# Kernel tuning notes

Hardware: AMD Instinct MI355X
Metric: run time of the kernel (lower is better)

The kernel has to match this reference:

```python
import jax, jax.numpy as jnp
import numpy as np

B, Z, NOBS = 16384, 64, 2
D = Z + NOBS  # update_mlp_in_size
H1, H2 = 16, 16
HC1, HC2 = 32, 32


def setup_inputs() -> dict:
    key = jax.random.key(0)
    ks = jax.random.split(key, 20)
    inp = {}
    inp['latents'] = jax.random.normal(ks[0], (B, Z), jnp.float32)
    inp['obs'] = jax.random.normal(ks[1], (B, NOBS), jnp.float32)
    # reparameterization noise (torch.randn_like equivalents, made explicit)
    inp['noise_update'] = jax.random.normal(ks[2], (B, D, Z), jnp.float32)
    inp['noise_global'] = jax.random.normal(ks[3], (B, Z), jnp.float32)
    # parameters
    inp['z_0'] = jax.random.normal(ks[4], (Z,), jnp.float32)
    inp['mult_u'] = jnp.ones((D, Z), jnp.float32)
    inp['logvar_u'] = jax.random.uniform(ks[5], (D, Z), jnp.float32, -3.0, -2.0)
    inp['mult_g'] = jnp.ones((Z,), jnp.float32)
    inp['logvar_g'] = jax.random.uniform(ks[6], (Z,), jnp.float32, -3.0, -2.0)
    # per-latent update MLPs, batched over Z
    s = lambda fan_in: 1.0 / np.sqrt(fan_in)
    inp['W1'] = jax.random.uniform(ks[7], (Z, D, H1), jnp.float32, -s(D), s(D))
    inp['b1'] = jax.random.uniform(ks[8], (Z, H1), jnp.float32, -s(D), s(D))
    inp['W2'] = jax.random.uniform(ks[9], (Z, H1, H2), jnp.float32, -s(H1), s(H1))
    inp['b2'] = jax.random.uniform(ks[10], (Z, H2), jnp.float32, -s(H1), s(H1))
    inp['W3'] = jax.random.uniform(ks[11], (Z, H2, 2), jnp.float32, -s(H2), s(H2))
    inp['b3'] = jax.random.uniform(ks[12], (Z, 2), jnp.float32, -s(H2), s(H2))
    # choice MLP (include_stimulus=False -> input dim Z)
    inp['Wc1'] = jax.random.uniform(ks[13], (Z, HC1), jnp.float32, -s(Z), s(Z))
    inp['bc1'] = jax.random.uniform(ks[14], (HC1,), jnp.float32, -s(Z), s(Z))
    inp['Wc2'] = jax.random.uniform(ks[15], (HC1, HC2), jnp.float32, -s(HC1), s(HC1))
    inp['bc2'] = jax.random.uniform(ks[16], (HC2,), jnp.float32, -s(HC1), s(HC1))
    inp['Wc3'] = jax.random.uniform(ks[17], (HC2, 2), jnp.float32, -s(HC2), s(HC2))
    inp['bc3'] = jax.random.uniform(ks[18], (2,), jnp.float32, -s(HC2), s(HC2))
    inp['t_0'] = 0  # False
    return inp


def reference(latents, obs, noise_update, noise_global, z_0, mult_u, logvar_u,
              mult_g, logvar_g, W1, b1, W2, b2, W3, b3,
              Wc1, bc1, Wc2, bc2, Wc3, bc3, t_0):
    lat = jnp.broadcast_to(z_0, latents.shape) if t_0 else latents  # [B,Z]
    x = jnp.concatenate([lat, obs], axis=-1)  # [B,D]
    # --- per-latent update bottlenecks, vectorized over Z ---
    var_u = jnp.exp(logvar_u)                      # [D,Z]
    mean_u = x[:, :, None] * mult_u[None]          # [B,D,Z]
    kld_u = -0.5 * jnp.sum(1.0 + logvar_u[None] - mean_u ** 2 - var_u[None], axis=1)  # [B,Z]
    x_tilde = noise_update * jnp.sqrt(var_u)[None] + mean_u  # [B,D,Z]
    # --- per-latent tiny MLPs, batched as grouped GEMMs ---
    h = jax.nn.relu(jnp.einsum('bdz,zdh->bzh', x_tilde, W1) + b1[None])
    h = jax.nn.relu(jnp.einsum('bzh,zhk->bzk', h, W2) + b2[None])
    o = jnp.einsum('bzk,zko->bzo', h, W3) + b3[None]          # [B,Z,2]
    u = o[..., 0]
    w = jax.nn.sigmoid(o[..., 1])
    new_latents = (1.0 - w) * lat + u * w          # gated update, [B,Z]
    # --- global bottleneck ---
    var_g = jnp.exp(logvar_g)
    mean_g = mult_g * new_latents
    kld_g = -0.5 * jnp.sum(1.0 + logvar_g - mean_g ** 2 - var_g, axis=-1)  # [B]
    z_tilde = noise_global * jnp.sqrt(var_g) + mean_g
    # --- choice MLP (no stimulus) ---
    y = jax.nn.relu(z_tilde @ Wc1 + bc1)
    y = jax.nn.relu(y @ Wc2 + bc2)
    y = y @ Wc3 + bc3                              # [B,2]
    return (y, z_tilde, kld_g, kld_u)
```

## Files before the change

kernel.cpp:

```cpp
#include <hip/hip_runtime.h>
#include <hip/hip_bf16.h>
#include <stdint.h>

#define BB 16384
#define ZZ 64
#define DD 66
#define NB 4
#define WPB 4

#define OFF_SVMU 0
#define OFF_C0U  8448
#define OFF_MG   8512
#define OFF_SVG  8576
#define OFF_C0G  8640

__global__ void prep_kernel(const float* __restrict__ mult_u, const float* __restrict__ logvar_u,
                            const float* __restrict__ mult_g, const float* __restrict__ logvar_g,
                            float* __restrict__ ws) {
  const int t = threadIdx.x;
  for (int i = t; i < DD*ZZ; i += 256) {
    ws[OFF_SVMU + 2*i]     = mult_u[i];
    ws[OFF_SVMU + 2*i + 1] = __expf(0.5f * logvar_u[i]);
  }
  if (t < ZZ) {
    float s = 0.f;
    for (int d = 0; d < DD; ++d) {
      const float lv = logvar_u[d*ZZ + t];
      s += 1.f + lv - __expf(lv);
    }
    ws[OFF_C0U + t] = -0.5f * s;
    ws[OFF_MG  + t] = mult_g[t];
    ws[OFF_SVG + t] = __expf(0.5f * logvar_g[t]);
  }
  if (t == 0) {
    float s = 0.f;
    for (int z = 0; z < ZZ; ++z) {
      const float lv = logvar_g[z];
      s += 1.f + lv - __expf(lv);
    }
    ws[OFF_C0G] = -0.5f * s;
  }
}

__global__ __launch_bounds__(256, 2)
void disrnn_main(const float* __restrict__ latents, const float* __restrict__ obs,
                 const float* __restrict__ noise_u, const float* __restrict__ noise_g,
                 const float* __restrict__ z0, const float* __restrict__ W1,
                 const float* __restrict__ b1, const float* __restrict__ W2,
                 const float* __restrict__ b2, const float* __restrict__ W3,
                 const float* __restrict__ b3,
                 const float* __restrict__ ws, const int* __restrict__ t0p,
                 float* __restrict__ out) {
  float* out_zt = out + BB*2;
  float* out_kg = out + BB*2 + BB*ZZ;
  float* out_ku = out + BB*2 + BB*ZZ + BB;

  __shared__ float x_lds[WPB][NB][68];
  __shared__ float red[WPB][NB][64];

  const int tid  = threadIdx.x;
  const int w    = tid >> 6;
  const int lane = tid & 63;
  const int b0   = (blockIdx.x * WPB + w) * NB;
  const int t0   = *t0p;

  const float c0u_l = ws[OFF_C0U + lane];
  const float mg_l  = ws[OFF_MG + lane];
  const float svg_l = ws[OFF_SVG + lane];
  const float c0g   = ws[OFF_C0G];
  const float b3_0  = b3[lane*2];
  const float b3_1  = b3[lane*2 + 1];
  const float2* __restrict__ svmu = (const float2*)(ws + OFF_SVMU);

#pragma unroll
  for (int i = 0; i < NB; ++i) {
    x_lds[w][i][lane] = t0 ? z0[lane] : latents[(b0 + i)*ZZ + lane];
    if (lane < 2) x_lds[w][i][ZZ + lane] = obs[(b0 + i)*2 + lane];
  }
  __syncthreads();

  float acc[NB][16], kacc[NB];
  {
    const float4* bp = reinterpret_cast<const float4*>(b1 + lane*16);
    float b1r[16];
#pragma unroll
    for (int q = 0; q < 4; ++q) {
      const float4 v = bp[q];
      b1r[4*q] = v.x; b1r[4*q+1] = v.y; b1r[4*q+2] = v.z; b1r[4*q+3] = v.w;
    }
#pragma unroll
    for (int i = 0; i < NB; ++i) {
      kacc[i] = 0.f;
#pragma unroll
      for (int h = 0; h < 16; ++h) acc[i][h] = b1r[h];
    }
  }

  for (int d = 0; d < DD; ++d) {
    const float2 sm = svmu[d*ZZ + lane];
    const float4* wp = reinterpret_cast<const float4*>(W1 + (lane*DD + d)*16);
    float wv[16];
#pragma unroll
    for (int q = 0; q < 4; ++q) {
      const float4 v = wp[q];
      wv[4*q] = v.x; wv[4*q+1] = v.y; wv[4*q+2] = v.z; wv[4*q+3] = v.w;
    }
#pragma unroll
    for (int i = 0; i < NB; ++i) {
      const float xv   = x_lds[w][i][d];
      const float mean = xv * sm.x;
      const float nv   = noise_u[((b0 + i)*DD + d)*ZZ + lane];
      const float xt   = fmaf(nv, sm.y, mean);
      kacc[i] = fmaf(mean, mean, kacc[i]);
#pragma unroll
      for (int h = 0; h < 16; ++h) acc[i][h] = fmaf(xt, wv[h], acc[i][h]);
    }
  }

  float h2[NB][16];
  {
    const float4* bp = reinterpret_cast<const float4*>(b2 + lane*16);
    float b2r[16];
#pragma unroll
    for (int q = 0; q < 4; ++q) {
      const float4 v = bp[q];
      b2r[4*q] = v.x; b2r[4*q+1] = v.y; b2r[4*q+2] = v.z; b2r[4*q+3] = v.w;
    }
#pragma unroll
    for (int i = 0; i < NB; ++i) {
#pragma unroll
      for (int h = 0; h < 16; ++h) acc[i][h] = fmaxf(acc[i][h], 0.f);
#pragma unroll
      for (int k = 0; k < 16; ++k) h2[i][k] = b2r[k];
    }
  }
  for (int h = 0; h < 16; ++h) {
    const float4* wp = reinterpret_cast<const float4*>(W2 + (lane*16 + h)*16);
    float wv[16];
#pragma unroll
    for (int q = 0; q < 4; ++q) {
      const float4 v = wp[q];
      wv[4*q] = v.x; wv[4*q+1] = v.y; wv[4*q+2] = v.z; wv[4*q+3] = v.w;
    }
#pragma unroll
    for (int i = 0; i < NB; ++i) {
      const float hv = acc[i][h];
#pragma unroll
      for (int k = 0; k < 16; ++k) h2[i][k] = fmaf(hv, wv[k], h2[i][k]);
    }
  }

  float w3r[32];
  {
    const float4* wp = reinterpret_cast<const float4*>(W3 + lane*32);
#pragma unroll
    for (int q = 0; q < 8; ++q) {
      const float4 v = wp[q];
      w3r[4*q] = v.x; w3r[4*q+1] = v.y; w3r[4*q+2] = v.z; w3r[4*q+3] = v.w;
    }
  }
#pragma unroll
  for (int i = 0; i < NB; ++i) {
    const int b = b0 + i;
    float o0 = b3_0, o1 = b3_1;
#pragma unroll
    for (int k = 0; k < 16; ++k) {
      const float hv = fmaxf(h2[i][k], 0.f);
      o0 = fmaf(hv, w3r[2*k], o0);
      o1 = fmaf(hv, w3r[2*k + 1], o1);
    }
    const float xl = x_lds[w][i][lane];
    const float wg = 1.f / (1.f + __expf(-o1));
    const float nl = fmaf(wg, o0 - xl, xl);
    const float tg = mg_l * nl;
    const float zt = fmaf(noise_g[b*ZZ + lane], svg_l, tg);
    out_zt[b*ZZ + lane] = zt;
    out_ku[b*ZZ + lane] = fmaf(0.5f, kacc[i], c0u_l);
    red[w][i][lane] = tg * tg;
  }
  __syncthreads();
  if (lane < NB) {
    float s = 0.f;
    for (int z = 0; z < ZZ; ++z) s += red[w][lane][z];
    out_kg[b0 + lane] = fmaf(0.5f, s, c0g);
  }
}

__global__ __launch_bounds__(256, 2)
void choice_kernel(const float* __restrict__ Wc1, const float* __restrict__ bc1,
                   const float* __restrict__ Wc2, const float* __restrict__ bc2,
                   const float* __restrict__ Wc3, const float* __restrict__ bc3,
                   float* __restrict__ out) {
  const float* zt_in = out + BB*2;
  float* out_y = out;

  __shared__ float zl[WPB][64];
  __shared__ float y1[WPB][32];
  __shared__ float y2[WPB][32];

  const int tid  = threadIdx.x;
  const int w    = tid >> 6;
  const int lane = tid & 63;
  const int b    = blockIdx.x * WPB + w;

  zl[w][lane] = zt_in[b*ZZ + lane];
  __syncthreads();
  if (lane < 32) {
    float a = bc1[lane];
    for (int z = 0; z < 64; ++z) a = fmaf(zl[w][z], Wc1[z*32 + lane], a);
    y1[w][lane] = fmaxf(a, 0.f);
  }
  __syncthreads();
  if (lane < 32) {
    float a = bc2[lane];
    for (int h = 0; h < 32; ++h) a = fmaf(y1[w][h], Wc2[h*32 + lane], a);
    y2[w][lane] = fmaxf(a, 0.f);
  }
  __syncthreads();
  if (lane == 0) {
    float s0 = bc3[0], s1 = bc3[1];
    for (int k = 0; k < 32; ++k) {
      s0 = fmaf(y2[w][k], Wc3[2*k], s0);
      s1 = fmaf(y2[w][k], Wc3[2*k + 1], s1);
    }
    out_y[b*2]     = s0;
    out_y[b*2 + 1] = s1;
  }
}

extern "C" void kernel_launch(void* const* d_in, const int* in_sizes, int n_in,
                              void* d_out, int out_size, void* d_ws, size_t ws_size,
                              hipStream_t stream) {
  const float* latents  = (const float*)d_in[0];
  const float* obs      = (const float*)d_in[1];
  const float* noise_u  = (const float*)d_in[2];
  const float* noise_g  = (const float*)d_in[3];
  const float* z0       = (const float*)d_in[4];
  const float* mult_u   = (const float*)d_in[5];
  const float* logvar_u = (const float*)d_in[6];
  const float* mult_g   = (const float*)d_in[7];
  const float* logvar_g = (const float*)d_in[8];
  const float* W1       = (const float*)d_in[9];
  const float* b1       = (const float*)d_in[10];
  const float* W2       = (const float*)d_in[11];
  const float* b2       = (const float*)d_in[12];
  const float* W3       = (const float*)d_in[13];
  const float* b3       = (const float*)d_in[14];
  const float* Wc1      = (const float*)d_in[15];
  const float* bc1      = (const float*)d_in[16];
  const float* Wc2      = (const float*)d_in[17];
  const float* bc2      = (const float*)d_in[18];
  const float* Wc3      = (const float*)d_in[19];
  const float* bc3      = (const float*)d_in[20];
  const int*  t0p       = (const int*)d_in[21];
  float* ws = (float*)d_ws;
  float* outp = (float*)d_out;

  prep_kernel<<<1, 256, 0, stream>>>(mult_u, logvar_u, mult_g, logvar_g, ws);
  disrnn_main<<<BB/(WPB*NB), 256, 0, stream>>>(latents, obs, noise_u, noise_g, z0,
                                               W1, b1, W2, b2, W3, b3,
                                               ws, t0p, outp);
  choice_kernel<<<BB/WPB, 256, 0, stream>>>(Wc1, bc1, Wc2, bc2, Wc3, bc3, outp);
}
```

Measured before the change: 620.0 us.

## Fuse choice MLP into main kernel and batch noise loads per chunk

The choice MLP is folded into the main kernel. Each block stages Wc1, Wc2 and Wc3 in LDS and computes y from z_tilde held in shared memory, which removes a kernel launch and the re-read of z_tilde from global memory. The first-layer loop now issues noise and scale loads for 4 d-values ahead of the FMAs, so more memory requests are in flight at once. The second-layer MLP is restructured per batch row to lower register pressure. The cost is more LDS per block, and the LDS reductions drop their block barriers and rely on wavefront-level execution.

```diff
diff --git a/kernel.cpp b/kernel.cpp
--- a/kernel.cpp
+++ b/kernel.cpp
@@ -1,5 +1,4 @@
 #include <hip/hip_runtime.h>
-#include <hip/hip_bf16.h>
 #include <stdint.h>
 
 #define BB 16384
@@ -49,14 +48,25 @@
                  const float* __restrict__ b1, const float* __restrict__ W2,
                  const float* __restrict__ b2, const float* __restrict__ W3,
                  const float* __restrict__ b3,
+                 const float* __restrict__ Wc1, const float* __restrict__ bc1,
+                 const float* __restrict__ Wc2, const float* __restrict__ bc2,
+                 const float* __restrict__ Wc3, const float* __restrict__ bc3,
                  const float* __restrict__ ws, const int* __restrict__ t0p,
                  float* __restrict__ out) {
+  float* out_y  = out;
   float* out_zt = out + BB*2;
   float* out_kg = out + BB*2 + BB*ZZ;
   float* out_ku = out + BB*2 + BB*ZZ + BB;
 
-  __shared__ float x_lds[WPB][NB][68];
-  __shared__ float red[WPB][NB][64];
+  __shared__ float s_x[WPB][NB][68];
+  __shared__ float s_red[WPB][NB][64];
+  __shared__ float s_zt[WPB][NB][64];
+  __shared__ float s_y1[WPB][2][2][32];
+  __shared__ float s_y2[WPB][2][2][32];
+  __shared__ float s_wc1[2048];
+  __shared__ float s_wc2[1024];
+  __shared__ float s_wc3[64];
+  __shared__ float s_bc1[32], s_bc2[32], s_bc3[2];
 
   const int tid  = threadIdx.x;
   const int w    = tid >> 6;
@@ -64,167 +74,185 @@
   const int b0   = (blockIdx.x * WPB + w) * NB;
   const int t0   = *t0p;
 
+  for (int idx = tid; idx < 2048; idx += 256) s_wc1[idx] = Wc1[idx];
+  for (int idx = tid; idx < 1024; idx += 256) s_wc2[idx] = Wc2[idx];
+  if (tid < 64) s_wc3[tid] = Wc3[tid];
+  if (tid < 32) { s_bc1[tid] = bc1[tid]; s_bc2[tid] = bc2[tid]; }
+  if (tid < 2)  s_bc3[tid] = bc3[tid];
+
+#pragma unroll
+  for (int i = 0; i < NB; ++i) {
+    s_x[w][i][lane] = t0 ? z0[lane] : latents[(b0 + i)*ZZ + lane];
+    if (lane < 2) s_x[w][i][ZZ + lane] = obs[(b0 + i)*2 + lane];
+  }
+  __syncthreads();
+
+  const float2* __restrict__ svmu = (const float2*)(ws + OFF_SVMU);
+
+  float acc[NB][16], kacc[NB];
+  {
+    const float4* bp = reinterpret_cast<const float4*>(b1 + lane*16);
+    float b1r[16];
+#pragma unroll
+    for (int q = 0; q < 4; ++q) {
+      const float4 v = bp[q];
+      b1r[4*q] = v.x; b1r[4*q+1] = v.y; b1r[4*q+2] = v.z; b1r[4*q+3] = v.w;
+    }
+#pragma unroll
+    for (int i = 0; i < NB; ++i) {
+      kacc[i] = 0.f;
+#pragma unroll
+      for (int h = 0; h < 16; ++h) acc[i][h] = b1r[h];
+    }
+  }
+
+  for (int c = 0; c < 16; ++c) {
+    const int d0 = c * 4;
+    float2 smb[4];
+    float  nvb[4][NB];
+#pragma unroll
+    for (int u = 0; u < 4; ++u) {
+      smb[u] = svmu[(d0 + u)*ZZ + lane];
+#pragma unroll
+      for (int i = 0; i < NB; ++i)
+        nvb[u][i] = noise_u[((b0 + i)*DD + d0 + u)*ZZ + lane];
+    }
+#pragma unroll
+    for (int u = 0; u < 4; ++u) {
+      const int d = d0 + u;
+      const float4* wp = reinterpret_cast<const float4*>(W1 + (lane*DD + d)*16);
+      float wv[16];
+#pragma unroll
+      for (int q = 0; q < 4; ++q) {
+        const float4 v = wp[q];
+        wv[4*q] = v.x; wv[4*q+1] = v.y; wv[4*q+2] = v.z; wv[4*q+3] = v.w;
+      }
+#pragma unroll
+      for (int i = 0; i < NB; ++i) {
+        const float xv   = s_x[w][i][d];
+        const float mean = xv * smb[u].x;
+        const float xt   = fmaf(nvb[u][i], smb[u].y, mean);
+        kacc[i] = fmaf(mean, mean, kacc[i]);
+#pragma unroll
+        for (int h = 0; h < 16; ++h) acc[i][h] = fmaf(xt, wv[h], acc[i][h]);
+      }
+    }
+  }
+  {
+    float2 smb[2];
+    float  nvb[2][NB];
+#pragma unroll
+    for (int u = 0; u < 2; ++u) {
+      smb[u] = svmu[(64 + u)*ZZ + lane];
+#pragma unroll
+      for (int i = 0; i < NB; ++i)
+        nvb[u][i] = noise_u[((b0 + i)*DD + 64 + u)*ZZ + lane];
+    }
+#pragma unroll
+    for (int u = 0; u < 2; ++u) {
+      const int d = 64 + u;
+      const float4* wp = reinterpret_cast<const float4*>(W1 + (lane*DD + d)*16);
+      float wv[16];
+#pragma unroll
+      for (int q = 0; q < 4; ++q) {
+        const float4 v = wp[q];
+        wv[4*q] = v.x; wv[4*q+1] = v.y; wv[4*q+2] = v.z; wv[4*q+3] = v.w;
+      }
+#pragma unroll
+      for (int i = 0; i < NB; ++i) {
+        const float xv   = s_x[w][i][d];
+        const float mean = xv * smb[u].x;
+        const float xt   = fmaf(nvb[u][i], smb[u].y, mean);
+        kacc[i] = fmaf(mean, mean, kacc[i]);
+#pragma unroll
+        for (int h = 0; h < 16; ++h) acc[i][h] = fmaf(xt, wv[h], acc[i][h]);
+      }
+    }
+  }
+
   const float c0u_l = ws[OFF_C0U + lane];
   const float mg_l  = ws[OFF_MG + lane];
   const float svg_l = ws[OFF_SVG + lane];
   const float c0g   = ws[OFF_C0G];
-  const float b3_0  = b3[lane*2];
-  const float b3_1  = b3[lane*2 + 1];
-  const float2* __restrict__ svmu = (const float2*)(ws + OFF_SVMU);
-
-#pragma unroll
-  for (int i = 0; i < NB; ++i) {
-    x_lds[w][i][lane] = t0 ? z0[lane] : latents[(b0 + i)*ZZ + lane];
-    if (lane < 2) x_lds[w][i][ZZ + lane] = obs[(b0 + i)*2 + lane];
-  }
-  __syncthreads();
-
-  float acc[NB][16], kacc[NB];
-  {
-    const float4* bp = reinterpret_cast<const float4*>(b1 + lane*16);
-    float b1r[16];
-#pragma unroll
-    for (int q = 0; q < 4; ++q) {
-      const float4 v = bp[q];
-      b1r[4*q] = v.x; b1r[4*q+1] = v.y; b1r[4*q+2] = v.z; b1r[4*q+3] = v.w;
-    }
-#pragma unroll
-    for (int i = 0; i < NB; ++i) {
-      kacc[i] = 0.f;
-#pragma unroll
-      for (int h = 0; h < 16; ++h) acc[i][h] = b1r[h];
-    }
-  }
-
-  for (int d = 0; d < DD; ++d) {
-    const float2 sm = svmu[d*ZZ + lane];
-    const float4* wp = reinterpret_cast<const float4*>(W1 + (lane*DD + d)*16);
-    float wv[16];
-#pragma unroll
-    for (int q = 0; q < 4; ++q) {
-      const float4 v = wp[q];
-      wv[4*q] = v.x; wv[4*q+1] = v.y; wv[4*q+2] = v.z; wv[4*q+3] = v.w;
-    }
-#pragma unroll
-    for (int i = 0; i < NB; ++i) {
-      const float xv   = x_lds[w][i][d];
-      const float mean = xv * sm.x;
-      const float nv   = noise_u[((b0 + i)*DD + d)*ZZ + lane];
-      const float xt   = fmaf(nv, sm.y, mean);
-      kacc[i] = fmaf(mean, mean, kacc[i]);
-#pragma unroll
-      for (int h = 0; h < 16; ++h) acc[i][h] = fmaf(xt, wv[h], acc[i][h]);
-    }
-  }
-
-  float h2[NB][16];
-  {
-    const float4* bp = reinterpret_cast<const float4*>(b2 + lane*16);
-    float b2r[16];
-#pragma unroll
-    for (int q = 0; q < 4; ++q) {
-      const float4 v = bp[q];
-      b2r[4*q] = v.x; b2r[4*q+1] = v.y; b2r[4*q+2] = v.z; b2r[4*q+3] = v.w;
-    }
-#pragma unroll
-    for (int i = 0; i < NB; ++i) {
-#pragma unroll
-      for (int h = 0; h < 16; ++h) acc[i][h] = fmaxf(acc[i][h], 0.f);
-#pragma unroll
-      for (int k = 0; k < 16; ++k) h2[i][k] = b2r[k];
-    }
-  }
-  for (int h = 0; h < 16; ++h) {
-    const float4* wp = reinterpret_cast<const float4*>(W2 + (lane*16 + h)*16);
-    float wv[16];
-#pragma unroll
-    for (int q = 0; q < 4; ++q) {
-      const float4 v = wp[q];
-      wv[4*q] = v.x; wv[4*q+1] = v.y; wv[4*q+2] = v.z; wv[4*q+3] = v.w;
-    }
-#pragma unroll
-    for (int i = 0; i < NB; ++i) {
-      const float hv = acc[i][h];
-#pragma unroll
-      for (int k = 0; k < 16; ++k) h2[i][k] = fmaf(hv, wv[k], h2[i][k]);
-    }
-  }
-
-  float w3r[32];
-  {
-    const float4* wp = reinterpret_cast<const float4*>(W3 + lane*32);
-#pragma unroll
-    for (int q = 0; q < 8; ++q) {
-      const float4 v = wp[q];
-      w3r[4*q] = v.x; w3r[4*q+1] = v.y; w3r[4*q+2] = v.z; w3r[4*q+3] = v.w;
-    }
-  }
 #pragma unroll
   for (int i = 0; i < NB; ++i) {
     const int b = b0 + i;
-    float o0 = b3_0, o1 = b3_1;
-#pragma unroll
-    for (int k = 0; k < 16; ++k) {
-      const float hv = fmaxf(h2[i][k], 0.f);
-      o0 = fmaf(hv, w3r[2*k], o0);
-      o1 = fmaf(hv, w3r[2*k + 1], o1);
-    }
-    const float xl = x_lds[w][i][lane];
+    float h2[16];
+    {
+      const float4* bp = reinterpret_cast<const float4*>(b2 + lane*16);
+#pragma unroll
+      for (int q = 0; q < 4; ++q) {
+        const float4 v = bp[q];
+        h2[4*q] = v.x; h2[4*q+1] = v.y; h2[4*q+2] = v.z; h2[4*q+3] = v.w;
+      }
+    }
+#pragma unroll
+    for (int h = 0; h < 16; ++h) {
+      const float hv = fmaxf(acc[i][h], 0.f);
+      const float4* wp = reinterpret_cast<const float4*>(W2 + (lane*16 + h)*16);
+#pragma unroll
+      for (int q = 0; q < 4; ++q) {
+        const float4 v = wp[q];
+        h2[4*q]   = fmaf(hv, v.x, h2[4*q]);
+        h2[4*q+1] = fmaf(hv, v.y, h2[4*q+1]);
+        h2[4*q+2] = fmaf(hv, v.z, h2[4*q+2]);
+        h2[4*q+3] = fmaf(hv, v.w, h2[4*q+3]);
+      }
+    }
+    float o0 = b3[lane*2], o1 = b3[lane*2 + 1];
+    {
+      const float4* wp3 = reinterpret_cast<const float4*>(W3 + lane*32);
+#pragma unroll
+      for (int q = 0; q < 8; ++q) {
+        const float4 v = wp3[q];
+        const float hv0 = fmaxf(h2[2*q],     0.f);
+        const float hv1 = fmaxf(h2[2*q + 1], 0.f);
+        o0 = fmaf(hv0, v.x, fmaf(hv1, v.z, o0));
+        o1 = fmaf(hv0, v.y, fmaf(hv1, v.w, o1));
+      }
+    }
+    const float xl = s_x[w][i][lane];
     const float wg = 1.f / (1.f + __expf(-o1));
     const float nl = fmaf(wg, o0 - xl, xl);
     const float tg = mg_l * nl;
     const float zt = fmaf(noise_g[b*ZZ + lane], svg_l, tg);
     out_zt[b*ZZ + lane] = zt;
     out_ku[b*ZZ + lane] = fmaf(0.5f, kacc[i], c0u_l);
-    red[w][i][lane] = tg * tg;
-  }
-  __syncthreads();
+    s_red[w][i][lane] = tg * tg;
+    s_zt[w][i][lane]  = zt;
+  }
+
   if (lane < NB) {
     float s = 0.f;
-    for (int z = 0; z < ZZ; ++z) s += red[w][lane][z];
+    for (int z = 0; z < ZZ; ++z) s += s_red[w][lane][z];
     out_kg[b0 + lane] = fmaf(0.5f, s, c0g);
   }
-}
-
-__global__ __launch_bounds__(256, 2)
-void choice_kernel(const float* __restrict__ Wc1, const float* __restrict__ bc1,
-                   const float* __restrict__ Wc2, const float* __restrict__ bc2,
-                   const float* __restrict__ Wc3, const float* __restrict__ bc3,
-                   float* __restrict__ out) {
-  const float* zt_in = out + BB*2;
-  float* out_y = out;
-
-  __shared__ float zl[WPB][64];
-  __shared__ float y1[WPB][32];
-  __shared__ float y2[WPB][32];
-
-  const int tid  = threadIdx.x;
-  const int w    = tid >> 6;
-  const int lane = tid & 63;
-  const int b    = blockIdx.x * WPB + w;
-
-  zl[w][lane] = zt_in[b*ZZ + lane];
-  __syncthreads();
-  if (lane < 32) {
-    float a = bc1[lane];
-    for (int z = 0; z < 64; ++z) a = fmaf(zl[w][z], Wc1[z*32 + lane], a);
-    y1[w][lane] = fmaxf(a, 0.f);
-  }
-  __syncthreads();
-  if (lane < 32) {
-    float a = bc2[lane];
-    for (int h = 0; h < 32; ++h) a = fmaf(y1[w][h], Wc2[h*32 + lane], a);
-    y2[w][lane] = fmaxf(a, 0.f);
-  }
-  __syncthreads();
-  if (lane == 0) {
-    float s0 = bc3[0], s1 = bc3[1];
-    for (int k = 0; k < 32; ++k) {
-      s0 = fmaf(y2[w][k], Wc3[2*k], s0);
-      s1 = fmaf(y2[w][k], Wc3[2*k + 1], s1);
-    }
-    out_y[b*2]     = s0;
-    out_y[b*2 + 1] = s1;
+
+#pragma unroll
+  for (int q = 0; q < 2; ++q) {
+    const int p = lane >> 5;
+    const int j = lane & 31;
+    const int i = 2*q + p;
+    float a0 = 0.f, a1 = 0.f;
+#pragma unroll 8
+    for (int z = 0; z < 64; z += 2) {
+      a0 = fmaf(s_zt[w][i][z],     s_wc1[z*32 + j],       a0);
+      a1 = fmaf(s_zt[w][i][z + 1], s_wc1[(z + 1)*32 + j], a1);
+    }
+    s_y1[w][q][p][j] = fmaxf(a0 + a1 + s_bc1[j], 0.f);
+    float c0v = 0.f, c1v = 0.f;
+#pragma unroll 8
+    for (int h = 0; h < 32; h += 2) {
+      c0v = fmaf(s_y1[w][q][p][h],     s_wc2[h*32 + j],       c0v);
+      c1v = fmaf(s_y1[w][q][p][h + 1], s_wc2[(h + 1)*32 + j], c1v);
+    }
+    s_y2[w][q][p][j] = fmaxf(c0v + c1v + s_bc2[j], 0.f);
+    if (lane < 4) {
+      const int pp = lane >> 1, o = lane & 1;
+      float s = s_bc3[o];
+      for (int k = 0; k < 32; ++k) s = fmaf(s_y2[w][q][pp][k], s_wc3[2*k + o], s);
+      out_y[(b0 + 2*q + pp)*2 + o] = s;
+    }
   }
 }
 
@@ -259,6 +287,6 @@
   prep_kernel<<<1, 256, 0, stream>>>(mult_u, logvar_u, mult_g, logvar_g, ws);
   disrnn_main<<<BB/(WPB*NB), 256, 0, stream>>>(latents, obs, noise_u, noise_g, z0,
                                                W1, b1, W2, b2, W3, b3,
+                                               Wc1, bc1, Wc2, bc2, Wc3, bc3,
                                                ws, t0p, outp);
-  choice_kernel<<<BB/WPB, 256, 0, stream>>>(Wc1, bc1, Wc2, bc2, Wc3, bc3, outp);
 }
```

New measurement: 1.425 ms. 2.3x slower.
